# Optimization experiments

Measured on AMD Instinct MI355X. Metric: run time of the kernel, lower is better.

Reference implementation:

```python
import jax, jax.numpy as jnp
import numpy as np

N, S, EMB, H = 4, 2048, 512, 8
D = EMB // H  # 64


def setup_inputs() -> dict:
    key = jax.random.key(0)
    ks = jax.random.split(key, 10)
    sc = 0.02
    return {
        "x": jax.random.normal(ks[0], (N, S, EMB), dtype=jnp.float32),
        "Wq": jax.random.normal(ks[1], (D, D), dtype=jnp.float32) * sc,
        "bq": jax.random.normal(ks[2], (D,), dtype=jnp.float32) * sc,
        "Wk": jax.random.normal(ks[3], (D, D), dtype=jnp.float32) * sc,
        "bk": jax.random.normal(ks[4], (D,), dtype=jnp.float32) * sc,
        "Wv": jax.random.normal(ks[5], (D, D), dtype=jnp.float32) * sc,
        "bv": jax.random.normal(ks[6], (D,), dtype=jnp.float32) * sc,
        "E": jax.random.normal(ks[7], (1, S, D), dtype=jnp.float32),
        "Wo": jax.random.normal(ks[8], (EMB, EMB), dtype=jnp.float32) * sc,
        "bo": jax.random.normal(ks[9], (EMB,), dtype=jnp.float32) * sc,
    }


def reference(x, Wq, bq, Wk, bk, Wv, bv, E, Wo, bo):
    n, s, emb = x.shape
    h, d = H, D
    xh = x.reshape(n, s, h, d)
    # per-head Linear projections (torch Linear: y = x @ W.T + b)
    q = xh @ Wq.T + bq  # [n,s,h,d]
    k = xh @ Wk.T + bk
    v = xh @ Wv.T + bv

    # QE = queries.transpose(1,2) @ E.transpose(1,2) -> [n,h,s,s]
    QE = jnp.einsum('nqhd,sd->nhqs', q, E[0])
    # _mask_positions: zero where triu(ones(S,S),1) flipped along columns == 1
    triu1 = jnp.triu(jnp.ones((s, s), dtype=bool), 1)
    QE = jnp.where(triu1[:, ::-1], 0.0, QE)
    # _skew: pad last dim on the left, reinterpret (s, s+1) as (s+1, s), drop first row
    padded = jnp.pad(QE, ((0, 0), (0, 0), (0, 0), (1, 0)))  # [n,h,s,s+1]
    Smat = padded.reshape(n, h, s + 1, s)[:, :, 1:, :]  # [n,h,s,s]

    qk = jnp.einsum('nqhd,nkhd->nhqk', q, k)
    # faithful to source: fill where mask==0 (lower triangle incl. diag) with -1e20
    qk = jnp.where(triu1, qk, jnp.float32(-1e20))
    attention = jax.nn.softmax(qk / (emb ** 0.5), axis=3) + Smat

    z = jnp.einsum('nhql,nlhd->nqhd', attention, v).reshape(n, s, h * d)
    return z @ Wo.T + bo


if __name__ == "__main__":
    out = reference(**setup_inputs())
    print(out.shape, out.dtype)
```

## Files before the change

kernel.cpp:

```cpp
#include <hip/hip_runtime.h>
#include <hip/hip_bf16.h>

#define S_LEN 2048
#define EMB   512
#define NH    8
#define DH    64
#define NB    4

typedef float f32x4  __attribute__((ext_vector_type(4)));
typedef short short8 __attribute__((ext_vector_type(8)));

__device__ __forceinline__ unsigned short f2bf_rn(float f) {
    return __builtin_bit_cast(unsigned short, __float2bfloat16(f));
}

__device__ __forceinline__ f32x4 mfma16(short8 a, short8 b, f32x4 c) {
    return __builtin_amdgcn_mfma_f32_16x16x32_bf16(a, b, c, 0, 0, 0);
}

__device__ __forceinline__ short8 frag_read(const unsigned short* lds, int row, int oct)
{
    const char* src = (const char*)lds + row * 128 + ((oct * 16) ^ ((row & 7) << 4));
    return *reinterpret_cast<const short8*>(src);
}

__device__ __forceinline__ int pinv(int k) {
    return (k & 32) + ((k >> 2) & 3) * 8 + (k & 3) + ((k & 16) >> 2);
}

__device__ __forceinline__ void stage_tile_f32(const float* __restrict__ g,
                                               int gstride, unsigned short* lds, int tid)
{
    #pragma unroll
    for (int c = tid; c < 512; c += 256) {
        const int r = c >> 3, s = c & 7;
        const float4* src = (const float4*)(g + (size_t)r * gstride + s * 8);
        const float4 a = src[0], b = src[1];
        short8 f;
        f[0] = (short)f2bf_rn(a.x); f[1] = (short)f2bf_rn(a.y);
        f[2] = (short)f2bf_rn(a.z); f[3] = (short)f2bf_rn(a.w);
        f[4] = (short)f2bf_rn(b.x); f[5] = (short)f2bf_rn(b.y);
        f[6] = (short)f2bf_rn(b.z); f[7] = (short)f2bf_rn(b.w);
        char* dst = (char*)lds + r * 128 + ((s * 16) ^ ((r & 7) << 4));
        *reinterpret_cast<short8*>(dst) = f;
    }
}

__device__ __forceinline__ void softmax_pack(const f32x4 C[4], bool diag, int ws, int og,
                                             int rowg, float& dsum, short8& pa0, short8& pa1)
{
    constexpr float SM_SCALE = 0.04419417382415922f;
    float rsum = 0.f;
    unsigned short pw[16];
    if (!diag) {
        #pragma unroll
        for (int t = 0; t < 4; ++t)
            #pragma unroll
            for (int r = 0; r < 4; ++r) {
                const float wv = __expf(C[t][r] * SM_SCALE);
                rsum += wv;
                pw[t * 4 + r] = f2bf_rn(wv);
            }
    } else {
        #pragma unroll
        for (int t = 0; t < 4; ++t)
            #pragma unroll
            for (int r = 0; r < 4; ++r) {
                const bool keep = (t > ws) || (t == ws && (og * 4 + r) > rowg);
                const float wv = keep ? __expf(C[t][r] * SM_SCALE) : 0.f;
                rsum += wv;
                pw[t * 4 + r] = f2bf_rn(wv);
            }
    }
    dsum += rsum;
    #pragma unroll
    for (int i = 0; i < 8; ++i) { pa0[i] = (short)pw[i]; pa1[i] = (short)pw[8 + i]; }
}

__global__ __launch_bounds__(256) void qkv_mfma(
    const float* __restrict__ x,
    const float* __restrict__ Wq, const float* __restrict__ bq,
    const float* __restrict__ Wk, const float* __restrict__ bk,
    const float* __restrict__ Wv, const float* __restrict__ bv,
    unsigned short* __restrict__ qg, unsigned short* __restrict__ kg,
    unsigned short* __restrict__ vg)
{
    __shared__ unsigned short w_lds[3][64 * 64];

    const int tid  = threadIdx.x;
    const int lane = tid & 63;
    const int w    = tid >> 6;
    const int rowg = lane & 15;
    const int og   = lane >> 4;

    stage_tile_f32(Wq, 64, w_lds[0], tid);
    stage_tile_f32(Wk, 64, w_lds[1], tid);
    stage_tile_f32(Wv, 64, w_lds[2], tid);

    float bias[3][4];
    #pragma unroll
    for (int t = 0; t < 4; ++t) {
        bias[0][t] = bq[16 * t + rowg];
        bias[1][t] = bk[16 * t + rowg];
        bias[2][t] = bv[16 * t + rowg];
    }

    const int m0 = blockIdx.x * 64 + 16 * w;
    const float* xr = x + (size_t)(m0 + rowg) * 64;
    const float4 a0 = *(const float4*)(xr + og * 8);
    const float4 a1 = *(const float4*)(xr + og * 8 + 4);
    const float4 a2 = *(const float4*)(xr + 32 + og * 8);
    const float4 a3 = *(const float4*)(xr + 32 + og * 8 + 4);
    short8 af0, af1;
    af0[0] = (short)f2bf_rn(a0.x); af0[1] = (short)f2bf_rn(a0.y);
    af0[2] = (short)f2bf_rn(a0.z); af0[3] = (short)f2bf_rn(a0.w);
    af0[4] = (short)f2bf_rn(a1.x); af0[5] = (short)f2bf_rn(a1.y);
    af0[6] = (short)f2bf_rn(a1.z); af0[7] = (short)f2bf_rn(a1.w);
    af1[0] = (short)f2bf_rn(a2.x); af1[1] = (short)f2bf_rn(a2.y);
    af1[2] = (short)f2bf_rn(a2.z); af1[3] = (short)f2bf_rn(a2.w);
    af1[4] = (short)f2bf_rn(a3.x); af1[5] = (short)f2bf_rn(a3.y);
    af1[6] = (short)f2bf_rn(a3.z); af1[7] = (short)f2bf_rn(a3.w);

    __syncthreads();

    f32x4 acc[3][4];
    #pragma unroll
    for (int m = 0; m < 3; ++m)
        #pragma unroll
        for (int t = 0; t < 4; ++t) {
            const float b = bias[m][t];
            acc[m][t] = (f32x4){b, b, b, b};
        }

    #pragma unroll
    for (int m = 0; m < 3; ++m)
        #pragma unroll
        for (int t = 0; t < 4; ++t) {
            acc[m][t] = mfma16(af0, frag_read(w_lds[m], 16 * t + rowg, og),     acc[m][t]);
            acc[m][t] = mfma16(af1, frag_read(w_lds[m], 16 * t + rowg, og + 4), acc[m][t]);
        }

    unsigned short* outp[3] = {qg, kg, vg};
    #pragma unroll
    for (int m = 0; m < 3; ++m)
        #pragma unroll
        for (int r = 0; r < 4; ++r) {
            const int mr = (blockIdx.x * 64 + 16 * w) + og * 4 + r;
            const int tk = mr >> 3, h = mr & 7;
            const int n = tk >> 11, s = tk & 2047;
            const size_t rowb = (((size_t)(n * NH + h)) * S_LEN + s) * 64;
            #pragma unroll
            for (int t = 0; t < 4; ++t)
                outp[m][rowb + 16 * t + rowg] = f2bf_rn(acc[m][t][r]);
        }
}

__global__ __launch_bounds__(256) void transpose_v(
    const unsigned short* __restrict__ v, unsigned short* __restrict__ vt)
{
    __shared__ unsigned short t_lds[64][72];
    const int bid = blockIdx.x;
    const int st = bid % (S_LEN / 64);
    const int nh = bid / (S_LEN / 64);
    const unsigned short* vp = v + ((size_t)nh * S_LEN + st * 64) * DH;
    unsigned short* vtp = vt + (size_t)nh * DH * S_LEN + st * 64;
    const int tid = threadIdx.x;
    #pragma unroll
    for (int c = tid; c < 512; c += 256) {
        const int r = c >> 3, s = c & 7;
        short8 xv = *reinterpret_cast<const short8*>(vp + r * DH + s * 8);
        #pragma unroll
        for (int i = 0; i < 8; ++i) t_lds[s * 8 + i][r] = (unsigned short)xv[i];
    }
    __syncthreads();
    #pragma unroll
    for (int c = tid; c < 512; c += 256) {
        const int d = c >> 3, sc = c & 7;
        const int cb = ((sc & 4) << 3) + (sc & 3) * 4;
        short8 y;
        #pragma unroll
        for (int i = 0; i < 8; ++i)
            y[i] = (short)t_lds[d][cb + (i & 3) + ((i & 4) << 2)];
        *reinterpret_cast<short8*>(vtp + (size_t)d * S_LEN + sc * 8) = y;
    }
}

__global__ __launch_bounds__(256) void prep_e(
    const float* __restrict__ E, unsigned short* __restrict__ eb)
{
    const int i = blockIdx.x * 256 + threadIdx.x;
    if (i >= S_LEN * DH) return;
    const int dlt = i >> 6, d = i & 63;
    eb[i] = f2bf_rn(E[(size_t)(S_LEN - 1 - dlt) * DH + d]);
}

__global__ __launch_bounds__(256) void attn_mfma(
    const unsigned short* __restrict__ qg,
    const unsigned short* __restrict__ kg,
    const unsigned short* __restrict__ vtg,
    const unsigned short* __restrict__ eg,
    unsigned short* __restrict__ z)
{
    __shared__ __align__(16) unsigned short smem[20480];

    constexpr float UNI = 1.0f / 2048.0f;

    const int nqt = S_LEN / 64;
    const int bid = blockIdx.x;
    const int qt  = (nqt - 1) - (bid >> 5);
    const int nh  = bid & 31;
    const int q0  = qt * 64;
    const size_t base = (size_t)nh * S_LEN * DH;
    const unsigned short* qp = qg + base;
    const unsigned short* kp = kg + base;
    const unsigned short* vp = vtg + base;

    const int tid  = threadIdx.x;
    const int lane = tid & 63;
    const int w    = tid >> 6;
    const int rowg = lane & 15;
    const int og   = lane >> 4;

    const int r0 = tid >> 3,  s0 = tid & 7;
    const int r1 = r0 + 32;
    const int ldsoff0 = r0 * 128 + ((s0 * 16) ^ ((r0 & 7) << 4));
    const int ldsoff1 = r1 * 128 + ((s0 * 16) ^ ((r1 & 7) << 4));
    const int ksrc0 = r0 * 64 + s0 * 8,    ksrc1 = r1 * 64 + s0 * 8;
    const int vsrc0 = r0 * S_LEN + s0 * 8, vsrc1 = r1 * S_LEN + s0 * 8;

    short8 kr0, kr1, vr0, vr1;

    short8 qa0, qa1;
    {
        const unsigned short* qr = qp + (size_t)(q0 + 16 * w + rowg) * DH + og * 8;
        qa0 = *reinterpret_cast<const short8*>(qr);
        qa1 = *reinterpret_cast<const short8*>(qr + 32);
    }

    const f32x4 zero4 = {0.f, 0.f, 0.f, 0.f};
    f32x4 accS[4], accR[4];
    #pragma unroll
    for (int t = 0; t < 4; ++t) { accS[t] = zero4; accR[t] = zero4; }
    float dsum = 0.f;

    kr0 = *(const short8*)(kp + (size_t)q0 * 64 + ksrc0);
    kr1 = *(const short8*)(kp + (size_t)q0 * 64 + ksrc1);
    vr0 = *(const short8*)(vp + q0 + vsrc0);
    vr1 = *(const short8*)(vp + q0 + vsrc1);
    *(short8*)((char*)smem + ldsoff0) = kr0;
    *(short8*)((char*)smem + ldsoff1) = kr1;
    *(short8*)((char*)(smem + 8192) + ldsoff0) = vr0;
    *(short8*)((char*)(smem + 8192) + ldsoff1) = vr1;
    __syncthreads();

    int cur = 0;
    for (int k0 = q0; k0 < S_LEN; k0 += 64) {
        const bool pf = (k0 + 64 < S_LEN);
        if (pf) {
            const unsigned short* kb = kp + (size_t)(k0 + 64) * 64;
            const unsigned short* vb = vp + (k0 + 64);
            kr0 = *(const short8*)(kb + ksrc0);
            kr1 = *(const short8*)(kb + ksrc1);
            vr0 = *(const short8*)(vb + vsrc0);
            vr1 = *(const short8*)(vb + vsrc1);
        }
        const unsigned short* klds = smem + cur * 4096;
        const unsigned short* vlds = smem + 8192 + cur * 4096;

        f32x4 C[4];
        #pragma unroll
        for (int t = 0; t < 4; ++t) {
            const short8 kf0 = frag_read(klds, 16 * t + rowg, og);
            const short8 kf1 = frag_read(klds, 16 * t + rowg, og + 4);
            C[t] = mfma16(kf1, qa1, mfma16(kf0, qa0, zero4));
        }
        short8 pa0, pa1;
        softmax_pack(C, k0 == q0, w, og, rowg, dsum, pa0, pa1);

        #pragma unroll
        for (int tt = 0; tt < 4; ++tt) {
            const short8 vf0 = frag_read(vlds, 16 * tt + rowg, og);
            const short8 vf1 = frag_read(vlds, 16 * tt + rowg, og + 4);
            accS[tt] = mfma16(pa1, vf1, mfma16(pa0, vf0, accS[tt]));
        }

        if (pf) {
            unsigned short* kn = smem + (cur ^ 1) * 4096;
            unsigned short* vn = smem + 8192 + (cur ^ 1) * 4096;
            *(short8*)((char*)kn + ldsoff0) = kr0;
            *(short8*)((char*)kn + ldsoff1) = kr1;
            *(short8*)((char*)vn + ldsoff0) = vr0;
            *(short8*)((char*)vn + ldsoff1) = vr1;
        }
        __syncthreads();
        cur ^= 1;
    }

    unsigned short* const ebuf = smem + 16384;
    const int jmax = q0 >> 6;

    kr0 = *(const short8*)(eg + ksrc0);
    kr1 = *(const short8*)(eg + ksrc1);
    vr0 = *(const short8*)(vp + q0 + vsrc0);
    vr1 = *(const short8*)(vp + q0 + vsrc1);
    {
        const short8 z8 = {0, 0, 0, 0, 0, 0, 0, 0};
        #pragma unroll
        for (int c2 = 0; c2 < 2; ++c2) {
            const int cc = lane + 64 * c2;
            const int r = 16 * w + (cc >> 3), sc = cc & 7;
            *reinterpret_cast<short8*>((char*)smem + r * 128 + sc * 16) = z8;
        }
    }
    *(short8*)((char*)ebuf + ldsoff0) = kr0;
    *(short8*)((char*)ebuf + ldsoff1) = kr1;
    *(short8*)((char*)(smem + 8192) + ldsoff0) = vr0;
    *(short8*)((char*)(smem + 8192) + ldsoff1) = vr1;
    __syncthreads();

    for (int j = 0; j <= jmax; ++j) {
        const bool pf = (j < jmax);
        if (pf) {
            const unsigned short* ebn = eg + (size_t)(j + 1) * 4096;
            const unsigned short* vbn = vp + (q0 - 64 * (j + 1));
            kr0 = *(const short8*)(ebn + ksrc0);
            kr1 = *(const short8*)(ebn + ksrc1);
            vr0 = *(const short8*)(vbn + vsrc0);
            vr1 = *(const short8*)(vbn + vsrc1);
        }
        const unsigned short* vlds = smem + 8192 + (j & 1) * 4096;

        f32x4 G[4];
        #pragma unroll
        for (int t = 0; t < 4; ++t)
            G[t] = mfma16(qa1, frag_read(ebuf, 16 * t + rowg, og + 4),
                   mfma16(qa0, frag_read(ebuf, 16 * t + rowg, og), zero4));

        unsigned short* pc = smem + (j & 1) * 4096;
        unsigned short* pn = smem + ((j + 1) & 1) * 4096;
        #pragma unroll
        for (int t = 0; t < 4; ++t) {
            const int c = 16 * t + rowg;
            #pragma unroll
            for (int r = 0; r < 4; ++r) {
                const int qq = 16 * w + og * 4 + r;
                float val = G[t][r];
                if (q0 + qq == S_LEN - 1) val += UNI;
                const unsigned short bv = f2bf_rn(val);
                const int swz = (qq & 7) << 4;
                if (c <= qq) {
                    const int p = pinv(qq - c);
                    *(unsigned short*)((char*)pc + qq * 128 + ((p * 2) ^ swz)) = bv;
                } else if (pf) {
                    const int p = pinv(qq - c + 64);
                    *(unsigned short*)((char*)pn + qq * 128 + ((p * 2) ^ swz)) = bv;
                }
            }
        }

        const short8 pb0 = frag_read(pc, 16 * w + rowg, og);
        const short8 pb1 = frag_read(pc, 16 * w + rowg, og + 4);
        #pragma unroll
        for (int tt = 0; tt < 4; ++tt) {
            const short8 vf0 = frag_read(vlds, 16 * tt + rowg, og);
            const short8 vf1 = frag_read(vlds, 16 * tt + rowg, og + 4);
            accR[tt] = mfma16(pb1, vf1, mfma16(pb0, vf0, accR[tt]));
        }

        __syncthreads();
        if (pf) {
            unsigned short* vn = smem + 8192 + ((j + 1) & 1) * 4096;
            *(short8*)((char*)ebuf + ldsoff0) = kr0;
            *(short8*)((char*)ebuf + ldsoff1) = kr1;
            *(short8*)((char*)vn + ldsoff0) = vr0;
            *(short8*)((char*)vn + ldsoff1) = vr1;
            __syncthreads();
        }
    }

    dsum += __shfl_xor(dsum, 16);
    dsum += __shfl_xor(dsum, 32);

    const int n = nh >> 3, h = nh & 7;
    const int qrow0 = q0 + 16 * w + og * 4;
    #pragma unroll
    for (int r = 0; r < 4; ++r) {
        const int qrow = qrow0 + r;
        const float dn = __shfl(dsum, og * 4 + r);
        const float inv = (qrow == S_LEN - 1) ? 0.f : 1.f / dn;
        #pragma unroll
        for (int t = 0; t < 4; ++t) {
            const float zv = accS[t][r] * inv + accR[t][r];
            z[((size_t)n * S_LEN + qrow) * EMB + h * DH + 16 * t + rowg] = f2bf_rn(zv);
        }
    }
}

__global__ __launch_bounds__(256) void outproj_mfma(
    const unsigned short* __restrict__ z,
    const float* __restrict__ Wo, const float* __restrict__ bo,
    float* __restrict__ out)
{
    __shared__ unsigned short wo_lds[64 * 64];

    const int tid  = threadIdx.x;
    const int lane = tid & 63;
    const int w    = tid >> 6;
    const int rowg = lane & 15;
    const int og   = lane >> 4;

    const int nob = EMB / 64;
    const int mb = blockIdx.x / nob;
    const int ob = blockIdx.x % nob;
    const int m0 = mb * 64 + 16 * w;
    const int o0 = ob * 64;

    f32x4 acc[4];
    #pragma unroll
    for (int t = 0; t < 4; ++t) {
        const float b = bo[o0 + 16 * t + rowg];
        acc[t] = (f32x4){b, b, b, b};
    }

    for (int k0 = 0; k0 < EMB; k0 += 64) {
        __syncthreads();
        stage_tile_f32(Wo + (size_t)o0 * EMB + k0, EMB, wo_lds, tid);
        __syncthreads();
        const unsigned short* zr = z + (size_t)(m0 + rowg) * EMB + k0;
        const short8 af0 = *reinterpret_cast<const short8*>(zr + og * 8);
        const short8 af1 = *reinterpret_cast<const short8*>(zr + 32 + og * 8);
        #pragma unroll
        for (int t = 0; t < 4; ++t) {
            acc[t] = mfma16(af0, frag_read(wo_lds, 16 * t + rowg, og),     acc[t]);
            acc[t] = mfma16(af1, frag_read(wo_lds, 16 * t + rowg, og + 4), acc[t]);
        }
    }

    #pragma unroll
    for (int r = 0; r < 4; ++r) {
        const size_t rowb = (size_t)(m0 + og * 4 + r) * EMB + o0;
        #pragma unroll
        for (int t = 0; t < 4; ++t)
            out[rowb + 16 * t + rowg] = acc[t][r];
    }
}

extern "C" void kernel_launch(void* const* d_in, const int* in_sizes, int n_in,
                              void* d_out, int out_size, void* d_ws, size_t ws_size,
                              hipStream_t stream) {
    const float* x  = (const float*)d_in[0];
    const float* Wq = (const float*)d_in[1];
    const float* bq = (const float*)d_in[2];
    const float* Wk = (const float*)d_in[3];
    const float* bk = (const float*)d_in[4];
    const float* Wv = (const float*)d_in[5];
    const float* bv = (const float*)d_in[6];
    const float* E  = (const float*)d_in[7];
    const float* Wo = (const float*)d_in[8];
    const float* bo = (const float*)d_in[9];
    float* out = (float*)d_out;

    const size_t per = (size_t)NB * NH * S_LEN * DH;
    unsigned short* qb  = (unsigned short*)d_ws;
    unsigned short* kb  = qb  + per;
    unsigned short* vb  = kb  + per;
    unsigned short* vtb = vb  + per;
    unsigned short* eb  = vtb + per;
    unsigned short* zb  = eb + (size_t)S_LEN * DH;

    qkv_mfma<<<(NB * S_LEN * NH) / 64, 256, 0, stream>>>(x, Wq, bq, Wk, bk, Wv, bv,
                                                         qb, kb, vb);
    transpose_v<<<NB * NH * (S_LEN / 64), 256, 0, stream>>>(vb, vtb);
    prep_e<<<(S_LEN * DH + 255) / 256, 256, 0, stream>>>(E, eb);
    attn_mfma<<<NB * NH * (S_LEN / 64), 256, 0, stream>>>(qb, kb, vtb, eb, zb);
    outproj_mfma<<<(NB * S_LEN / 64) * (EMB / 64), 256, 0, stream>>>(zb, Wo, bo, out);
}
```

Before: 123.3 us.

## Software-pipeline PV MMA behind next QK tile with triple-buffered V

The main attention loop is restructured so the P·V MFMAs for the previous tile run right after the current tile's QK MFMAs, with softmax moved after the LDS stores. V now rotates through three LDS buffers (one reusing the ebuf region) so the overlap is safe, and a drain step after the loop finishes the last tile. s_setprio hints raise wave priority around the MFMA blocks in both loops, and the row-sum reduction is split into four partial sums to shorten the dependency chain. The aim is to hide exp and softmax latency behind matrix work, at the cost of more live registers and an extra barrier.

```diff
diff --git a/kernel.cpp b/kernel.cpp
--- a/kernel.cpp
+++ b/kernel.cpp
@@ -50,29 +50,35 @@
                                              int rowg, float& dsum, short8& pa0, short8& pa1)
 {
     constexpr float SM_SCALE = 0.04419417382415922f;
-    float rsum = 0.f;
+    float rs[4];
     unsigned short pw[16];
     if (!diag) {
         #pragma unroll
-        for (int t = 0; t < 4; ++t)
+        for (int t = 0; t < 4; ++t) {
+            float a = 0.f;
             #pragma unroll
             for (int r = 0; r < 4; ++r) {
                 const float wv = __expf(C[t][r] * SM_SCALE);
-                rsum += wv;
+                a += wv;
                 pw[t * 4 + r] = f2bf_rn(wv);
             }
+            rs[t] = a;
+        }
     } else {
         #pragma unroll
-        for (int t = 0; t < 4; ++t)
+        for (int t = 0; t < 4; ++t) {
+            float a = 0.f;
             #pragma unroll
             for (int r = 0; r < 4; ++r) {
                 const bool keep = (t > ws) || (t == ws && (og * 4 + r) > rowg);
                 const float wv = keep ? __expf(C[t][r] * SM_SCALE) : 0.f;
-                rsum += wv;
+                a += wv;
                 pw[t * 4 + r] = f2bf_rn(wv);
             }
-    }
-    dsum += rsum;
+            rs[t] = a;
+        }
+    }
+    dsum += (rs[0] + rs[1]) + (rs[2] + rs[3]);
     #pragma unroll
     for (int i = 0; i < 8; ++i) { pa0[i] = (short)pw[i]; pa1[i] = (short)pw[8 + i]; }
 }
@@ -243,6 +249,7 @@
     for (int t = 0; t < 4; ++t) { accS[t] = zero4; accR[t] = zero4; }
     float dsum = 0.f;
 
+    const int T = (S_LEN - q0) >> 6;
     kr0 = *(const short8*)(kp + (size_t)q0 * 64 + ksrc0);
     kr1 = *(const short8*)(kp + (size_t)q0 * 64 + ksrc1);
     vr0 = *(const short8*)(vp + q0 + vsrc0);
@@ -253,20 +260,20 @@
     *(short8*)((char*)(smem + 8192) + ldsoff1) = vr1;
     __syncthreads();
 
-    int cur = 0;
-    for (int k0 = q0; k0 < S_LEN; k0 += 64) {
-        const bool pf = (k0 + 64 < S_LEN);
+    short8 pa0, pa1;
+    for (int ti = 0; ti < T; ++ti) {
+        const bool pf = (ti + 1 < T);
         if (pf) {
-            const unsigned short* kb = kp + (size_t)(k0 + 64) * 64;
-            const unsigned short* vb = vp + (k0 + 64);
+            const unsigned short* kb = kp + (size_t)(q0 + (ti + 1) * 64) * 64;
+            const unsigned short* vb = vp + (q0 + (ti + 1) * 64);
             kr0 = *(const short8*)(kb + ksrc0);
             kr1 = *(const short8*)(kb + ksrc1);
             vr0 = *(const short8*)(vb + vsrc0);
             vr1 = *(const short8*)(vb + vsrc1);
         }
-        const unsigned short* klds = smem + cur * 4096;
-        const unsigned short* vlds = smem + 8192 + cur * 4096;
-
+        const unsigned short* klds = smem + (ti & 1) * 4096;
+
+        __builtin_amdgcn_s_setprio(1);
         f32x4 C[4];
         #pragma unroll
         for (int t = 0; t < 4; ++t) {
@@ -274,27 +281,40 @@
             const short8 kf1 = frag_read(klds, 16 * t + rowg, og + 4);
             C[t] = mfma16(kf1, qa1, mfma16(kf0, qa0, zero4));
         }
-        short8 pa0, pa1;
-        softmax_pack(C, k0 == q0, w, og, rowg, dsum, pa0, pa1);
-
-        #pragma unroll
-        for (int tt = 0; tt < 4; ++tt) {
-            const short8 vf0 = frag_read(vlds, 16 * tt + rowg, og);
-            const short8 vf1 = frag_read(vlds, 16 * tt + rowg, og + 4);
-            accS[tt] = mfma16(pa1, vf1, mfma16(pa0, vf0, accS[tt]));
-        }
+        if (ti > 0) {
+            const unsigned short* vprev = smem + 8192 + ((ti + 2) % 3) * 4096;
+            #pragma unroll
+            for (int tt = 0; tt < 4; ++tt) {
+                const short8 vf0 = frag_read(vprev, 16 * tt + rowg, og);
+                const short8 vf1 = frag_read(vprev, 16 * tt + rowg, og + 4);
+                accS[tt] = mfma16(pa1, vf1, mfma16(pa0, vf0, accS[tt]));
+            }
+        }
+        __builtin_amdgcn_s_setprio(0);
 
         if (pf) {
-            unsigned short* kn = smem + (cur ^ 1) * 4096;
-            unsigned short* vn = smem + 8192 + (cur ^ 1) * 4096;
+            unsigned short* kn = smem + ((ti + 1) & 1) * 4096;
+            unsigned short* vn = smem + 8192 + ((ti + 1) % 3) * 4096;
             *(short8*)((char*)kn + ldsoff0) = kr0;
             *(short8*)((char*)kn + ldsoff1) = kr1;
             *(short8*)((char*)vn + ldsoff0) = vr0;
             *(short8*)((char*)vn + ldsoff1) = vr1;
         }
+        softmax_pack(C, ti == 0, w, og, rowg, dsum, pa0, pa1);
         __syncthreads();
-        cur ^= 1;
-    }
+    }
+    {
+        const unsigned short* vprev = smem + 8192 + ((T + 2) % 3) * 4096;
+        __builtin_amdgcn_s_setprio(1);
+        #pragma unroll
+        for (int tt = 0; tt < 4; ++tt) {
+            const short8 vf0 = frag_read(vprev, 16 * tt + rowg, og);
+            const short8 vf1 = frag_read(vprev, 16 * tt + rowg, og + 4);
+            accS[tt] = mfma16(pa1, vf1, mfma16(pa0, vf0, accS[tt]));
+        }
+        __builtin_amdgcn_s_setprio(0);
+    }
+    __syncthreads();
 
     unsigned short* const ebuf = smem + 16384;
     const int jmax = q0 >> 6;
@@ -330,11 +350,13 @@
         }
         const unsigned short* vlds = smem + 8192 + (j & 1) * 4096;
 
+        __builtin_amdgcn_s_setprio(1);
         f32x4 G[4];
         #pragma unroll
         for (int t = 0; t < 4; ++t)
             G[t] = mfma16(qa1, frag_read(ebuf, 16 * t + rowg, og + 4),
                    mfma16(qa0, frag_read(ebuf, 16 * t + rowg, og), zero4));
+        __builtin_amdgcn_s_setprio(0);
 
         unsigned short* pc = smem + (j & 1) * 4096;
         unsigned short* pn = smem + ((j + 1) & 1) * 4096;
@@ -360,12 +382,14 @@
 
         const short8 pb0 = frag_read(pc, 16 * w + rowg, og);
         const short8 pb1 = frag_read(pc, 16 * w + rowg, og + 4);
+        __builtin_amdgcn_s_setprio(1);
         #pragma unroll
         for (int tt = 0; tt < 4; ++tt) {
             const short8 vf0 = frag_read(vlds, 16 * tt + rowg, og);
             const short8 vf1 = frag_read(vlds, 16 * tt + rowg, og + 4);
             accR[tt] = mfma16(pb1, vf1, mfma16(pb0, vf0, accR[tt]));
         }
+        __builtin_amdgcn_s_setprio(0);
 
         __syncthreads();
         if (pf) {
```

Result: faster. 102.5 us (-16.9%).
